# Kernel optimization log

Measured on AMD Instinct MI355X. Metric: run time of the kernel, lower is better.

## Reference

```python
import jax, jax.numpy as jnp
import numpy as np

N_NODES = 50000
N_EDGES = 800000
N_GRAPHS = 64
NEG_SLOPE = 0.2  # PyG GATConv default leaky_relu slope
EPS = 1e-16      # PyG softmax denominator epsilon


def gat_conv(x, W, a_src, a_dst, bias, src, dst, n_nodes):
    """PyG GATConv (heads=1, concat=True, self-loops already appended).
    x: [N, F_in], W: [F_in, H*F], a_src/a_dst: [H, F], bias: [H*F]."""
    H, F = a_src.shape
    h = (x @ W).reshape(-1, H, F)                      # [N, H, F]
    alpha_src = jnp.einsum('nhf,hf->nh', h, a_src)     # [N, H]
    alpha_dst = jnp.einsum('nhf,hf->nh', h, a_dst)     # [N, H]
    e = jax.nn.leaky_relu(alpha_src[src] + alpha_dst[dst], NEG_SLOPE)  # [E, H]
    # segment softmax over incoming edges of each destination node
    e_max = jax.ops.segment_max(e, dst, num_segments=n_nodes)          # [N, H]
    e_exp = jnp.exp(e - e_max[dst])
    denom = jax.ops.segment_sum(e_exp, dst, num_segments=n_nodes)      # [N, H]
    alpha = e_exp / (denom[dst] + EPS)                                 # [E, H]
    msg = alpha[:, :, None] * h[src]                                   # [E, H, F]
    out = jax.ops.segment_sum(msg, dst, num_segments=n_nodes)          # [N, H, F]
    return out.reshape(-1, H * F) + bias


def global_mean_pool(x, batch, n_graphs):
    s = jax.ops.segment_sum(x, batch, num_segments=n_graphs)
    cnt = jax.ops.segment_sum(jnp.ones((x.shape[0],), x.dtype), batch, num_segments=n_graphs)
    return s / jnp.maximum(cnt, 1.0)[:, None]


def setup_inputs() -> dict:
    key = jax.random.key(0)
    ks = jax.random.split(key, 10)
    d_in, d_h, d_out, L, H = 128, 128, 10, 3, 1
    x = jax.random.normal(ks[0], (N_NODES, d_in), dtype=jnp.float32)
    edge_index = jax.random.randint(ks[1], (2, N_EDGES), 0, N_NODES, dtype=jnp.int32)
    edge_attr = jax.random.normal(ks[2], (N_EDGES, 4), dtype=jnp.float32)
    batch = jnp.sort(jax.random.randint(ks[3], (N_NODES,), 0, N_GRAPHS, dtype=jnp.int32))
    s0 = 1.0 / np.sqrt(d_in)
    sh = 1.0 / np.sqrt(d_h)
    return {
        'x': x,
        'edge_index': edge_index,
        'edge_attr': edge_attr,
        'batch': batch,
        'W0': jax.random.normal(ks[4], (d_in, d_h), dtype=jnp.float32) * s0,
        'b0': jnp.zeros((d_h,), jnp.float32),
        'Wc': jax.random.normal(ks[5], (L, d_h, H * d_h), dtype=jnp.float32) * sh,
        'att_src': jax.random.normal(ks[6], (L, H, d_h), dtype=jnp.float32) * sh,
        'att_dst': jax.random.normal(ks[7], (L, H, d_h), dtype=jnp.float32) * sh,
        'bc': jnp.zeros((L, H * d_h), jnp.float32),
        'W1': jax.random.normal(ks[8], (d_h, d_out), dtype=jnp.float32) * sh,
        'b1': jnp.zeros((d_out,), jnp.float32),
    }


def reference(x, edge_index, edge_attr, batch, W0, b0, Wc, att_src, att_dst, bc, W1, b1):
    n = x.shape[0]
    # GATConv default add_self_loops=True
    loops = jnp.arange(n, dtype=edge_index.dtype)
    src = jnp.concatenate([edge_index[0], loops])
    dst = jnp.concatenate([edge_index[1], loops])
    # dropout p=0 / eval mode -> identity
    h = jax.nn.relu(x @ W0 + b0)
    for i in range(Wc.shape[0]):
        h = jax.nn.relu(gat_conv(h, Wc[i], att_src[i], att_dst[i], bc[i], src, dst, n))
    pooled = global_mean_pool(h, batch, N_GRAPHS)   # [B, d_h]
    return pooled @ W1 + b1                          # [B, d_out]
```

## Files before the change

kernel.cpp:

```cpp
#include <hip/hip_runtime.h>
#include <hip/hip_bf16.h>
#include <hip/hip_fp16.h>
#include <hip/hip_fp8.h>

#define NN 50000
#define NE 800000
#define NG 64
#define DH 128

#define SEG 64
#define GEMMB 512
#define GEMMW (GEMMB * 4)
#define CST 136
#define CSTB 136
#define SMEM_BYTES 17408
#define NPAIR (NN / 2)
#define WTB 256
#define INITB ((NN + 255) / 256)
#define EPT 8
#define SCATB ((NE + 256 * EPT - 1) / (256 * EPT))

#if defined(__has_builtin)
# if __has_builtin(__builtin_amdgcn_cvt_pk_f32_fp8) && __has_builtin(__builtin_amdgcn_cvt_pk_fp8_f32)
#  define HW_FP8 1
# endif
#endif

typedef __bf16 bfx8 __attribute__((ext_vector_type(8)));
typedef float  f32x4 __attribute__((ext_vector_type(4)));
typedef float  f32x8 __attribute__((ext_vector_type(8)));

__device__ __forceinline__ ushort f2b(float f) {
    unsigned b = __float_as_uint(f);
    b += 0x7fff + ((b >> 16) & 1);
    return (ushort)(b >> 16);
}
__device__ __forceinline__ float b2f(ushort s) {
    return __uint_as_float((unsigned)s << 16);
}
__device__ __forceinline__ unsigned pk2(float a, float b) {
    return (unsigned)f2b(a) | ((unsigned)f2b(b) << 16);
}

__device__ __forceinline__ unsigned f2fp8(float v) {
    v = fminf(fmaxf(v, -448.f), 448.f);
#ifdef HW_FP8
    return (unsigned)__builtin_amdgcn_cvt_pk_fp8_f32(v, v, 0, false) & 0xFFu;
#else
    __hip_fp8_e4m3 t(v);
    return (unsigned)*(const unsigned char*)&t;
#endif
}
__device__ __forceinline__ void fp8x4_up(unsigned u, float* o) {
#ifdef HW_FP8
    auto lo = __builtin_amdgcn_cvt_pk_f32_fp8((int)u, false);
    auto hi = __builtin_amdgcn_cvt_pk_f32_fp8((int)u, true);
    o[0] = lo[0]; o[1] = lo[1]; o[2] = hi[0]; o[3] = hi[1];
#else
    #pragma unroll
    for (int k = 0; k < 4; ++k) {
        unsigned char c = (u >> (8 * k)) & 0xFF;
        o[k] = float(*(const __hip_fp8_e4m3*)&c);
    }
#endif
}

__launch_bounds__(256)
__global__ void k_misc(const float* __restrict__ W0, const float* __restrict__ Wc,
                       ushort* __restrict__ Wt, int* __restrict__ cur,
                       ushort* __restrict__ csr) {
    int t = threadIdx.x;
    if (blockIdx.x < WTB) {
        int i = blockIdx.x * 256 + t;
        int m = i >> 14;
        int r = i & 16383;
        int k = r >> 7, n = r & 127;
        const float* src = (m == 0) ? W0 : (Wc + (size_t)(m - 1) * DH * DH);
        Wt[(size_t)m * DH * DH + n * DH + k] = f2b(src[r]);
        return;
    }
    int n = (blockIdx.x - WTB) * 256 + t;
    if (n < NN) {
        cur[n] = (n << 6) + 1;
        csr[(size_t)n << 6] = (ushort)n;
    }
}

__launch_bounds__(256)
__global__ void k_scatter(const int* __restrict__ ei, int* __restrict__ cur,
                          ushort* __restrict__ csr) {
    int base = blockIdx.x * (256 * EPT) + threadIdx.x;
    int d[EPT], s[EPT], slot[EPT];
    #pragma unroll
    for (int j = 0; j < EPT; ++j) {
        int e = base + j * 256;
        d[j] = (e < NE) ? ei[NE + e] : -1;
    }
    #pragma unroll
    for (int j = 0; j < EPT; ++j) {
        int e = base + j * 256;
        s[j] = (e < NE) ? ei[e] : 0;
    }
    #pragma unroll
    for (int j = 0; j < EPT; ++j)
        if (d[j] >= 0) slot[j] = atomicAdd(&cur[d[j]], 1);
    #pragma unroll
    for (int j = 0; j < EPT; ++j)
        if (d[j] >= 0 && slot[j] < (d[j] << 6) + SEG) csr[slot[j]] = (ushort)s[j];
}

template<bool AF32, bool DOTS, bool OUTFP8>
__device__ __forceinline__ void gemm_body(char* smem, int gblk,
        const void* __restrict__ Av, const ushort* __restrict__ Wt,
        const float* __restrict__ bias, void* __restrict__ C, int relu,
        const float* __restrict__ avs, const float* __restrict__ avd,
        float* __restrict__ asrc, float* __restrict__ adst) {
    const int NT = NN / 16;
    int tid = threadIdx.x;
    int lane = tid & 63;
    int mrow = lane & 15;
    int quad = lane >> 4;
    int wid = (gblk * 256 + tid) >> 6;

    bfx8 b[4][8];
    #pragma unroll
    for (int ks = 0; ks < 4; ++ks) {
        int k0 = ks * 32 + quad * 8;
        #pragma unroll
        for (int t = 0; t < 8; ++t)
            b[ks][t] = *(const bfx8*)(Wt + (size_t)(t * 16 + mrow) * DH + k0);
    }
    float av[8], dv[8];
    if (DOTS) {
        #pragma unroll
        for (int t = 0; t < 8; ++t) {
            av[t] = avs[t * 16 + mrow];
            dv[t] = avd[t * 16 + mrow];
        }
    }

    for (int tile = wid; tile < NT; tile += GEMMW) {
        int row0 = tile * 16;
        int arow = row0 + mrow;

        bfx8 a[4];
        if (AF32) {
            f32x8 af[4];
            #pragma unroll
            for (int ks = 0; ks < 4; ++ks)
                af[ks] = *(const f32x8*)((const float*)Av + (size_t)arow * DH + ks * 32 + quad * 8);
            #pragma unroll
            for (int ks = 0; ks < 4; ++ks) {
                union { ushort s[8]; bfx8 v; } u;
                #pragma unroll
                for (int j = 0; j < 8; ++j) u.s[j] = f2b(af[ks][j]);
                a[ks] = u.v;
            }
        } else {
            #pragma unroll
            for (int ks = 0; ks < 4; ++ks)
                a[ks] = *(const bfx8*)((const ushort*)Av + (size_t)arow * DH + ks * 32 + quad * 8);
        }

        f32x4 acc[8];
        #pragma unroll
        for (int t = 0; t < 8; ++t)
            #pragma unroll
            for (int r = 0; r < 4; ++r) acc[t][r] = 0.f;

        #pragma unroll
        for (int ks = 0; ks < 4; ++ks)
            #pragma unroll
            for (int t = 0; t < 8; ++t)
                acc[t] = __builtin_amdgcn_mfma_f32_16x16x32_bf16(a[ks], b[ks][t], acc[t], 0, 0, 0);

        if (OUTFP8) {
            uchar* my = (uchar*)smem + (tid >> 6) * 16 * CSTB;
            #pragma unroll
            for (int t = 0; t < 8; ++t) {
                int col = t * 16 + mrow;
                float bv = bias ? bias[col] : 0.f;
                #pragma unroll
                for (int r = 0; r < 4; ++r) {
                    float v = acc[t][r] + bv;
                    if (relu) v = fmaxf(v, 0.f);
                    my[(quad * 4 + r) * CSTB + col] = (uchar)f2fp8(v);
                }
            }
            #pragma unroll
            for (int i = 0; i < 4; ++i) {
                int idx = i * 64 + lane;
                int row = idx >> 4;
                int c8 = idx & 15;
                uint2 u = *(const uint2*)(my + row * CSTB + c8 * 8);
                *(uint2*)((uchar*)C + (size_t)(row0 + row) * DH + c8 * 8) = u;
            }
        } else {
            ushort* my = (ushort*)smem + (tid >> 6) * 16 * CST;
            #pragma unroll
            for (int t = 0; t < 8; ++t) {
                int col = t * 16 + mrow;
                float bv = bias ? bias[col] : 0.f;
                #pragma unroll
                for (int r = 0; r < 4; ++r) {
                    float v = acc[t][r] + bv;
                    if (relu) v = fmaxf(v, 0.f);
                    my[(quad * 4 + r) * CST + col] = f2b(v);
                }
            }
            #pragma unroll
            for (int i = 0; i < 4; ++i) {
                int idx = i * 64 + lane;
                int row = idx >> 4;
                int c16 = idx & 15;
                uint4 u = *(const uint4*)(my + row * CST + c16 * 8);
                *(uint4*)((ushort*)C + (size_t)(row0 + row) * DH + c16 * 8) = u;
            }
        }

        if (DOTS) {
            int orow = row0 + quad * 4;
            #pragma unroll
            for (int r = 0; r < 4; ++r) {
                float ps = 0.f, pd = 0.f;
                #pragma unroll
                for (int t = 0; t < 8; ++t) {
                    ps += acc[t][r] * av[t];
                    pd += acc[t][r] * dv[t];
                }
                #pragma unroll
                for (int off = 1; off < 16; off <<= 1) {
                    ps += __shfl_xor(ps, off);
                    pd += __shfl_xor(pd, off);
                }
                if (mrow == 0) {
                    asrc[orow + r] = ps;
                    adst[orow + r] = pd;
                }
            }
        }
    }
}

__launch_bounds__(256)
__global__ void k_gemm1(const float* __restrict__ x, const ushort* __restrict__ Wt,
                        const float* __restrict__ b0, ushort* __restrict__ hB) {
    __shared__ char smem[SMEM_BYTES];
    gemm_body<true, false, false>(smem, blockIdx.x, x, Wt, b0, hB, 1,
                                  nullptr, nullptr, nullptr, nullptr);
}

__launch_bounds__(256)
__global__ void k_gemmdots(const ushort* __restrict__ hB, const ushort* __restrict__ Wt,
                           uchar* __restrict__ hA,
                           const float* __restrict__ avs, const float* __restrict__ avd,
                           float* __restrict__ asrc, float* __restrict__ adst) {
    __shared__ char smem[SMEM_BYTES];
    gemm_body<false, true, true>(smem, blockIdx.x, hB, Wt, nullptr, hA, 0,
                                 avs, avd, asrc, adst);
}

__device__ __forceinline__ void aggr_one(int wid, int lane,
        const uchar* __restrict__ h8, const float* __restrict__ asrc,
        const float* __restrict__ adst, const int* __restrict__ cur,
        const ushort* __restrict__ csr,
        const float* __restrict__ bias, ushort* __restrict__ hout) {
    int start = wid << 6;
    int cnt = min(cur[wid] - start, SEG);
    float ad = adst[wid];

    int s = csr[start + lane];
    float e = -1e30f;
    if (lane < cnt) {
        float t = asrc[s] + ad;
        e = fmaxf(t, 0.f) + 0.2f * fminf(t, 0.f);
    }
    float m = e;
    #pragma unroll
    for (int off = 32; off; off >>= 1) m = fmaxf(m, __shfl_xor(m, off));
    float w = (lane < cnt) ? __expf(e - m) : 0.f;
    float dsum = w;
    #pragma unroll
    for (int off = 32; off; off >>= 1) dsum += __shfl_xor(dsum, off);

    int g = lane >> 4, fidx = lane & 15;
    float acc[8];
    #pragma unroll
    for (int k = 0; k < 8; ++k) acc[k] = 0.f;

    int steps = (cnt + 3) >> 2;
    const uint2* hp = (const uint2*)h8;
    for (int j = 0; j < steps; ++j) {
        int e0 = j * 4 + g;
        float w0 = __shfl(w, e0);
        int   s0 = __shfl(s, e0);
        uint2 u0 = hp[(size_t)s0 * 16 + fidx];
        float v[8];
        fp8x4_up(u0.x, v); fp8x4_up(u0.y, v + 4);
        #pragma unroll
        for (int k = 0; k < 8; ++k) acc[k] += w0 * v[k];
    }
    #pragma unroll
    for (int k = 0; k < 8; ++k) {
        acc[k] += __shfl_xor(acc[k], 16);
        acc[k] += __shfl_xor(acc[k], 32);
    }
    if (g == 0) {
        float inv = 1.f / (dsum + 1e-16f);
        const float4* bp = (const float4*)bias;
        float4 b0 = bp[fidx * 2], b1 = bp[fidx * 2 + 1];
        uint4 o;
        o.x = pk2(fmaxf(acc[0] * inv + b0.x, 0.f), fmaxf(acc[1] * inv + b0.y, 0.f));
        o.y = pk2(fmaxf(acc[2] * inv + b0.z, 0.f), fmaxf(acc[3] * inv + b0.w, 0.f));
        o.z = pk2(fmaxf(acc[4] * inv + b1.x, 0.f), fmaxf(acc[5] * inv + b1.y, 0.f));
        o.w = pk2(fmaxf(acc[6] * inv + b1.z, 0.f), fmaxf(acc[7] * inv + b1.w, 0.f));
        ((uint4*)hout)[(size_t)wid * 16 + fidx] = o;
    }
}

__launch_bounds__(256)
__global__ void k_aggr(const uchar* __restrict__ h8, const float* __restrict__ asrc,
                       const float* __restrict__ adst, const int* __restrict__ cur,
                       const ushort* __restrict__ csr,
                       const float* __restrict__ bias, ushort* __restrict__ hout) {
    int pid = (blockIdx.x * blockDim.x + threadIdx.x) >> 6;
    int lane = threadIdx.x & 63;
    if (pid >= NPAIR) return;
    int half = lane >> 5, hl = lane & 31;
    int nd = pid * 2 + half;
    int start = nd << 6;

    int cnt = min(cur[nd] - start, SEG);
    int cother = __shfl_xor(cnt, 32);
    if (max(cnt, cother) <= 32) {
        float ad = adst[nd];
        int s = csr[start + hl];
        float e = -1e30f;
        if (hl < cnt) {
            float t = asrc[s] + ad;
            e = fmaxf(t, 0.f) + 0.2f * fminf(t, 0.f);
        }
        float m = e;
        #pragma unroll
        for (int off = 16; off; off >>= 1) m = fmaxf(m, __shfl_xor(m, off));
        float w = (hl < cnt) ? __expf(e - m) : 0.f;
        float dsum = w;
        #pragma unroll
        for (int off = 16; off; off >>= 1) dsum += __shfl_xor(dsum, off);

        int g = hl >> 4, fidx = hl & 15;
        int lbase = half * 32;
        float acc[8];
        #pragma unroll
        for (int k = 0; k < 8; ++k) acc[k] = 0.f;

        int steps = (cnt + 1) >> 1;
        const uint2* hp = (const uint2*)h8;
        int j = 0;
        for (; j + 3 < steps; j += 4) {
            int   e0 = j * 2 + g,       e1 = e0 + 2, e2 = e0 + 4, e3 = e0 + 6;
            float w0 = __shfl(w, lbase + e0), w1 = __shfl(w, lbase + e1);
            float w2 = __shfl(w, lbase + e2), w3 = __shfl(w, lbase + e3);
            int   s0 = __shfl(s, lbase + e0), s1 = __shfl(s, lbase + e1);
            int   s2 = __shfl(s, lbase + e2), s3 = __shfl(s, lbase + e3);
            uint2 u0 = hp[(size_t)s0 * 16 + fidx];
            uint2 u1 = hp[(size_t)s1 * 16 + fidx];
            uint2 u2 = hp[(size_t)s2 * 16 + fidx];
            uint2 u3 = hp[(size_t)s3 * 16 + fidx];
            float v[8];
            fp8x4_up(u0.x, v); fp8x4_up(u0.y, v + 4);
            #pragma unroll
            for (int k = 0; k < 8; ++k) acc[k] += w0 * v[k];
            fp8x4_up(u1.x, v); fp8x4_up(u1.y, v + 4);
            #pragma unroll
            for (int k = 0; k < 8; ++k) acc[k] += w1 * v[k];
            fp8x4_up(u2.x, v); fp8x4_up(u2.y, v + 4);
            #pragma unroll
            for (int k = 0; k < 8; ++k) acc[k] += w2 * v[k];
            fp8x4_up(u3.x, v); fp8x4_up(u3.y, v + 4);
            #pragma unroll
            for (int k = 0; k < 8; ++k) acc[k] += w3 * v[k];
        }
        for (; j < steps; ++j) {
            int   e0 = j * 2 + g;
            float w0 = __shfl(w, lbase + e0);
            int   s0 = __shfl(s, lbase + e0);
            uint2 u0 = hp[(size_t)s0 * 16 + fidx];
            float v[8];
            fp8x4_up(u0.x, v); fp8x4_up(u0.y, v + 4);
            #pragma unroll
            for (int k = 0; k < 8; ++k) acc[k] += w0 * v[k];
        }
        #pragma unroll
        for (int k = 0; k < 8; ++k) acc[k] += __shfl_xor(acc[k], 16);
        if (g == 0) {
            float inv = 1.f / (dsum + 1e-16f);
            const float4* bp = (const float4*)bias;
            float4 b0 = bp[fidx * 2], b1 = bp[fidx * 2 + 1];
            uint4 o;
            o.x = pk2(fmaxf(acc[0] * inv + b0.x, 0.f), fmaxf(acc[1] * inv + b0.y, 0.f));
            o.y = pk2(fmaxf(acc[2] * inv + b0.z, 0.f), fmaxf(acc[3] * inv + b0.w, 0.f));
            o.z = pk2(fmaxf(acc[4] * inv + b1.x, 0.f), fmaxf(acc[5] * inv + b1.y, 0.f));
            o.w = pk2(fmaxf(acc[6] * inv + b1.z, 0.f), fmaxf(acc[7] * inv + b1.w, 0.f));
            ((uint4*)hout)[(size_t)nd * 16 + fidx] = o;
        }
        return;
    }

    aggr_one(pid * 2,     lane, h8, asrc, adst, cur, csr, bias, hout);
    aggr_one(pid * 2 + 1, lane, h8, asrc, adst, cur, csr, bias, hout);
}

__launch_bounds__(256)
__global__ void k_pool(const ushort* __restrict__ h, const int* __restrict__ batch,
                       float* __restrict__ gsum, int* __restrict__ gcnt) {
    int slot = threadIdx.x >> 7;
    int f = threadIdx.x & 127;
    int n0 = blockIdx.x * 64;
    int n1 = min(n0 + 64, NN);
    int first = n0 + slot;
    if (first >= n1) return;
    int g0 = batch[n0], g1 = batch[n1 - 1];
    if (g0 == g1) {
        float acc = 0.f;
        for (int nd = first; nd < n1; nd += 2)
            acc += b2f(h[(size_t)nd * DH + f]);
        atomicAdd(&gsum[g0 * DH + f], acc);
        if (f == 0 && slot == 0) atomicAdd(&gcnt[g0], n1 - n0);
        return;
    }
    float acc = 0.f; int run = 0;
    int gcur = batch[first];
    for (int nd = first; nd < n1; nd += 2) {
        int g = batch[nd];
        if (g != gcur) {
            atomicAdd(&gsum[gcur * DH + f], acc);
            if (f == 0) atomicAdd(&gcnt[gcur], run);
            acc = 0.f; run = 0; gcur = g;
        }
        acc += b2f(h[(size_t)nd * DH + f]);
        run += 1;
    }
    atomicAdd(&gsum[gcur * DH + f], acc);
    if (f == 0) atomicAdd(&gcnt[gcur], run);
}

__global__ void k_final(const float* __restrict__ gsum, const int* __restrict__ gcnt,
                        const float* __restrict__ W1, const float* __restrict__ b1,
                        float* __restrict__ out) {
    int t = threadIdx.x;
    if (t >= NG * 10) return;
    int g = t / 10, o = t % 10;
    float inv = 1.f / fmaxf((float)gcnt[g], 1.f);
    float acc = 0.f;
    for (int f = 0; f < DH; ++f) acc += gsum[g * DH + f] * W1[f * 10 + o];
    out[t] = acc * inv + b1[o];
}

extern "C" void kernel_launch(void* const* d_in, const int* in_sizes, int n_in,
                              void* d_out, int out_size, void* d_ws, size_t ws_size,
                              hipStream_t stream) {
    const float* x       = (const float*)d_in[0];
    const int*   ei      = (const int*)d_in[1];
    const int*   batch   = (const int*)d_in[3];
    const float* W0      = (const float*)d_in[4];
    const float* b0      = (const float*)d_in[5];
    const float* Wc      = (const float*)d_in[6];
    const float* att_src = (const float*)d_in[7];
    const float* att_dst = (const float*)d_in[8];
    const float* bc      = (const float*)d_in[9];
    const float* W1      = (const float*)d_in[10];
    const float* b1      = (const float*)d_in[11];
    float* out = (float*)d_out;

    char* ws = (char*)d_ws;
    size_t off = 0;
    auto alloc = [&](size_t bytes) {
        void* p = ws + off;
        off += (bytes + 255) & ~(size_t)255;
        return p;
    };
    uchar*    hA     = (uchar*)alloc((size_t)NN * DH);
    ushort*   hB     = (ushort*)alloc((size_t)NN * DH * 2);
    ushort*   Wt     = (ushort*)alloc((size_t)4 * DH * DH * 2);
    ushort*   csr    = (ushort*)alloc((size_t)NN * SEG * 2);
    int*      cur    = (int*)alloc((size_t)NN * 4);
    float*    asrc   = (float*)alloc(NN * 4);
    float*    adst   = (float*)alloc(NN * 4);
    float*    gsum   = (float*)alloc(NG * DH * 4);
    int*      gcnt   = (int*)alloc(NG * 4);

    hipMemsetAsync(csr, 0, (size_t)NN * SEG * 2, stream);
    hipMemsetAsync(gsum, 0, NG * DH * 4 + 256, stream);

    k_misc<<<WTB + INITB, 256, 0, stream>>>(W0, Wc, Wt, cur, csr);
    k_scatter<<<SCATB, 256, 0, stream>>>(ei, cur, csr);
    k_gemm1<<<GEMMB, 256, 0, stream>>>(x, Wt, b0, hB);

    for (int l = 0; l < 3; ++l) {
        k_gemmdots<<<GEMMB, 256, 0, stream>>>(hB, Wt + (size_t)(l + 1) * DH * DH, hA,
                                              att_src + l * DH, att_dst + l * DH,
                                              asrc, adst);
        k_aggr<<<(NPAIR + 3) / 4, 256, 0, stream>>>(hA, asrc, adst, cur, csr,
                                                    bc + l * DH, hB);
    }

    k_pool<<<(NN + 63) / 64, 256, 0, stream>>>(hB, batch, gsum, gcnt);
    k_final<<<1, NG * 10, 0, stream>>>(gsum, gcnt, W1, b1, out);
}
```

Before: 306.1 us.

## Fuse front-end init, scatter and first GEMM into one kernel; deepen gather unroll

Merges weight conversion, self-loop init, edge scatter and the first GEMM into a single launch with block-range dispatch. It removes the dependency on a cur-init pass by zeroing cur via memset and storing relative slots. The first GEMM converts fp32 W0 on the fly with strided loads. The aggregation gather loop gains an 8-wide unrolled batch to issue more loads in flight, at the cost of more registers.

```diff
diff --git a/kernel.cpp b/kernel.cpp
--- a/kernel.cpp
+++ b/kernel.cpp
@@ -15,10 +15,11 @@
 #define CSTB 136
 #define SMEM_BYTES 17408
 #define NPAIR (NN / 2)
-#define WTB 256
-#define INITB ((NN + 255) / 256)
 #define EPT 8
 #define SCATB ((NE + 256 * EPT - 1) / (256 * EPT))
+#define WCB 192
+#define INITB ((NN + 255) / 256)
+#define FRONTB (SCATB + GEMMB + WCB + INITB)
 
 #if defined(__has_builtin)
 # if __has_builtin(__builtin_amdgcn_cvt_pk_f32_fp8) && __has_builtin(__builtin_amdgcn_cvt_pk_fp8_f32)
@@ -65,53 +66,9 @@
 #endif
 }
 
-__launch_bounds__(256)
-__global__ void k_misc(const float* __restrict__ W0, const float* __restrict__ Wc,
-                       ushort* __restrict__ Wt, int* __restrict__ cur,
-                       ushort* __restrict__ csr) {
-    int t = threadIdx.x;
-    if (blockIdx.x < WTB) {
-        int i = blockIdx.x * 256 + t;
-        int m = i >> 14;
-        int r = i & 16383;
-        int k = r >> 7, n = r & 127;
-        const float* src = (m == 0) ? W0 : (Wc + (size_t)(m - 1) * DH * DH);
-        Wt[(size_t)m * DH * DH + n * DH + k] = f2b(src[r]);
-        return;
-    }
-    int n = (blockIdx.x - WTB) * 256 + t;
-    if (n < NN) {
-        cur[n] = (n << 6) + 1;
-        csr[(size_t)n << 6] = (ushort)n;
-    }
-}
-
-__launch_bounds__(256)
-__global__ void k_scatter(const int* __restrict__ ei, int* __restrict__ cur,
-                          ushort* __restrict__ csr) {
-    int base = blockIdx.x * (256 * EPT) + threadIdx.x;
-    int d[EPT], s[EPT], slot[EPT];
-    #pragma unroll
-    for (int j = 0; j < EPT; ++j) {
-        int e = base + j * 256;
-        d[j] = (e < NE) ? ei[NE + e] : -1;
-    }
-    #pragma unroll
-    for (int j = 0; j < EPT; ++j) {
-        int e = base + j * 256;
-        s[j] = (e < NE) ? ei[e] : 0;
-    }
-    #pragma unroll
-    for (int j = 0; j < EPT; ++j)
-        if (d[j] >= 0) slot[j] = atomicAdd(&cur[d[j]], 1);
-    #pragma unroll
-    for (int j = 0; j < EPT; ++j)
-        if (d[j] >= 0 && slot[j] < (d[j] << 6) + SEG) csr[slot[j]] = (ushort)s[j];
-}
-
-template<bool AF32, bool DOTS, bool OUTFP8>
+template<bool AF32, bool BF32, bool DOTS, bool OUTFP8>
 __device__ __forceinline__ void gemm_body(char* smem, int gblk,
-        const void* __restrict__ Av, const ushort* __restrict__ Wt,
+        const void* __restrict__ Av, const void* __restrict__ Wp,
         const float* __restrict__ bias, void* __restrict__ C, int relu,
         const float* __restrict__ avs, const float* __restrict__ avd,
         float* __restrict__ asrc, float* __restrict__ adst) {
@@ -123,12 +80,29 @@
     int wid = (gblk * 256 + tid) >> 6;
 
     bfx8 b[4][8];
-    #pragma unroll
-    for (int ks = 0; ks < 4; ++ks) {
-        int k0 = ks * 32 + quad * 8;
-        #pragma unroll
-        for (int t = 0; t < 8; ++t)
-            b[ks][t] = *(const bfx8*)(Wt + (size_t)(t * 16 + mrow) * DH + k0);
+    if (BF32) {
+        const float* W = (const float*)Wp;
+        #pragma unroll
+        for (int ks = 0; ks < 4; ++ks) {
+            int k0 = ks * 32 + quad * 8;
+            #pragma unroll
+            for (int t = 0; t < 8; ++t) {
+                int n = t * 16 + mrow;
+                union { ushort s[8]; bfx8 v; } u;
+                #pragma unroll
+                for (int j = 0; j < 8; ++j) u.s[j] = f2b(W[(size_t)(k0 + j) * DH + n]);
+                b[ks][t] = u.v;
+            }
+        }
+    } else {
+        const ushort* Wt = (const ushort*)Wp;
+        #pragma unroll
+        for (int ks = 0; ks < 4; ++ks) {
+            int k0 = ks * 32 + quad * 8;
+            #pragma unroll
+            for (int t = 0; t < 8; ++t)
+                b[ks][t] = *(const bfx8*)(Wt + (size_t)(t * 16 + mrow) * DH + k0);
+        }
     }
     float av[8], dv[8];
     if (DOTS) {
@@ -243,11 +217,51 @@
 }
 
 __launch_bounds__(256)
-__global__ void k_gemm1(const float* __restrict__ x, const ushort* __restrict__ Wt,
+__global__ void k_front(const int* __restrict__ ei, int* __restrict__ cur,
+                        ushort* __restrict__ csr,
+                        const float* __restrict__ Wc, ushort* __restrict__ Wt,
+                        const float* __restrict__ x, const float* __restrict__ W0,
                         const float* __restrict__ b0, ushort* __restrict__ hB) {
     __shared__ char smem[SMEM_BYTES];
-    gemm_body<true, false, false>(smem, blockIdx.x, x, Wt, b0, hB, 1,
-                                  nullptr, nullptr, nullptr, nullptr);
+    int t = threadIdx.x;
+    unsigned bid = blockIdx.x;
+    if (bid < SCATB) {
+        int base = bid * (256 * EPT) + t;
+        int d[EPT], s[EPT], slot[EPT];
+        #pragma unroll
+        for (int j = 0; j < EPT; ++j) {
+            int e = base + j * 256;
+            d[j] = (e < NE) ? ei[NE + e] : -1;
+        }
+        #pragma unroll
+        for (int j = 0; j < EPT; ++j) {
+            int e = base + j * 256;
+            s[j] = (e < NE) ? ei[e] : 0;
+        }
+        #pragma unroll
+        for (int j = 0; j < EPT; ++j)
+            if (d[j] >= 0) slot[j] = atomicAdd(&cur[d[j]], 1);
+        #pragma unroll
+        for (int j = 0; j < EPT; ++j)
+            if (d[j] >= 0 && slot[j] < SEG - 1)
+                csr[((size_t)d[j] << 6) + 1 + slot[j]] = (ushort)s[j];
+        return;
+    }
+    if (bid < SCATB + GEMMB) {
+        gemm_body<true, true, false, false>(smem, bid - SCATB, x, W0, b0, hB, 1,
+                                            nullptr, nullptr, nullptr, nullptr);
+        return;
+    }
+    if (bid < SCATB + GEMMB + WCB) {
+        int i = (bid - SCATB - GEMMB) * 256 + t;
+        int m = i >> 14;
+        int r = i & 16383;
+        int k = r >> 7, n = r & 127;
+        Wt[(size_t)(m + 1) * DH * DH + n * DH + k] = f2b(Wc[(size_t)m * DH * DH + r]);
+        return;
+    }
+    int n = (bid - SCATB - GEMMB - WCB) * 256 + t;
+    if (n < NN) csr[(size_t)n << 6] = (ushort)n;
 }
 
 __launch_bounds__(256)
@@ -256,8 +270,8 @@
                            const float* __restrict__ avs, const float* __restrict__ avd,
                            float* __restrict__ asrc, float* __restrict__ adst) {
     __shared__ char smem[SMEM_BYTES];
-    gemm_body<false, true, true>(smem, blockIdx.x, hB, Wt, nullptr, hA, 0,
-                                 avs, avd, asrc, adst);
+    gemm_body<false, false, true, true>(smem, blockIdx.x, hB, Wt, nullptr, hA, 0,
+                                        avs, avd, asrc, adst);
 }
 
 __device__ __forceinline__ void aggr_one(int wid, int lane,
@@ -266,7 +280,7 @@
         const ushort* __restrict__ csr,
         const float* __restrict__ bias, ushort* __restrict__ hout) {
     int start = wid << 6;
-    int cnt = min(cur[wid] - start, SEG);
+    int cnt = min(cur[wid] + 1, SEG);
     float ad = adst[wid];
 
     int s = csr[start + lane];
@@ -330,7 +344,7 @@
     int nd = pid * 2 + half;
     int start = nd << 6;
 
-    int cnt = min(cur[nd] - start, SEG);
+    int cnt = min(cur[nd] + 1, SEG);
     int cother = __shfl_xor(cnt, 32);
     if (max(cnt, cother) <= 32) {
         float ad = adst[nd];
@@ -357,29 +371,41 @@
         int steps = (cnt + 1) >> 1;
         const uint2* hp = (const uint2*)h8;
         int j = 0;
+        for (; j + 7 < steps; j += 8) {
+            float ww[8]; int ss[8]; uint2 uu[8];
+            #pragma unroll
+            for (int q = 0; q < 8; ++q) {
+                int eq = (j + q) * 2 + g;
+                ww[q] = __shfl(w, lbase + eq);
+                ss[q] = __shfl(s, lbase + eq);
+            }
+            #pragma unroll
+            for (int q = 0; q < 8; ++q) uu[q] = hp[(size_t)ss[q] * 16 + fidx];
+            #pragma unroll
+            for (int q = 0; q < 8; ++q) {
+                float v[8];
+                fp8x4_up(uu[q].x, v); fp8x4_up(uu[q].y, v + 4);
+                #pragma unroll
+                for (int k = 0; k < 8; ++k) acc[k] += ww[q] * v[k];
+            }
+        }
         for (; j + 3 < steps; j += 4) {
-            int   e0 = j * 2 + g,       e1 = e0 + 2, e2 = e0 + 4, e3 = e0 + 6;
-            float w0 = __shfl(w, lbase + e0), w1 = __shfl(w, lbase + e1);
-            float w2 = __shfl(w, lbase + e2), w3 = __shfl(w, lbase + e3);
-            int   s0 = __shfl(s, lbase + e0), s1 = __shfl(s, lbase + e1);
-            int   s2 = __shfl(s, lbase + e2), s3 = __shfl(s, lbase + e3);
-            uint2 u0 = hp[(size_t)s0 * 16 + fidx];
-            uint2 u1 = hp[(size_t)s1 * 16 + fidx];
-            uint2 u2 = hp[(size_t)s2 * 16 + fidx];
-            uint2 u3 = hp[(size_t)s3 * 16 + fidx];
-            float v[8];
-            fp8x4_up(u0.x, v); fp8x4_up(u0.y, v + 4);
-            #pragma unroll
-            for (int k = 0; k < 8; ++k) acc[k] += w0 * v[k];
-            fp8x4_up(u1.x, v); fp8x4_up(u1.y, v + 4);
-            #pragma unroll
-            for (int k = 0; k < 8; ++k) acc[k] += w1 * v[k];
-            fp8x4_up(u2.x, v); fp8x4_up(u2.y, v + 4);
-            #pragma unroll
-            for (int k = 0; k < 8; ++k) acc[k] += w2 * v[k];
-            fp8x4_up(u3.x, v); fp8x4_up(u3.y, v + 4);
-            #pragma unroll
-            for (int k = 0; k < 8; ++k) acc[k] += w3 * v[k];
+            float ww[4]; int ss[4]; uint2 uu[4];
+            #pragma unroll
+            for (int q = 0; q < 4; ++q) {
+                int eq = (j + q) * 2 + g;
+                ww[q] = __shfl(w, lbase + eq);
+                ss[q] = __shfl(s, lbase + eq);
+            }
+            #pragma unroll
+            for (int q = 0; q < 4; ++q) uu[q] = hp[(size_t)ss[q] * 16 + fidx];
+            #pragma unroll
+            for (int q = 0; q < 4; ++q) {
+                float v[8];
+                fp8x4_up(uu[q].x, v); fp8x4_up(uu[q].y, v + 4);
+                #pragma unroll
+                for (int k = 0; k < 8; ++k) acc[k] += ww[q] * v[k];
+            }
         }
         for (; j < steps; ++j) {
             int   e0 = j * 2 + g;
@@ -490,12 +516,10 @@
     float*    gsum   = (float*)alloc(NG * DH * 4);
     int*      gcnt   = (int*)alloc(NG * 4);
 
-    hipMemsetAsync(csr, 0, (size_t)NN * SEG * 2, stream);
+    hipMemsetAsync(csr, 0, (size_t)NN * SEG * 2 + (size_t)NN * 4, stream);
     hipMemsetAsync(gsum, 0, NG * DH * 4 + 256, stream);
 
-    k_misc<<<WTB + INITB, 256, 0, stream>>>(W0, Wc, Wt, cur, csr);
-    k_scatter<<<SCATB, 256, 0, stream>>>(ei, cur, csr);
-    k_gemm1<<<GEMMB, 256, 0, stream>>>(x, Wt, b0, hB);
+    k_front<<<FRONTB, 256, 0, stream>>>(ei, cur, csr, Wc, Wt, x, W0, b0, hB);
 
     for (int l = 0; l < 3; ++l) {
         k_gemmdots<<<GEMMB, 256, 0, stream>>>(hB, Wt + (size_t)(l + 1) * DH * DH, hA,
```

After: 305.2 us. About the same (-0.3%).

## Fuse CSR init and scatter into one prep kernel; widen aggr gathers to 16B

Applied to the files above, without the earlier changes.

Merges the weight-transpose/init kernel and the edge-scatter kernel into a single launch. It does this by zeroing the per-node counters with the existing memset, so they no longer need a separate init pass, and writing edges at slot+1 after the self-loop. The aggregation fast path now has each lane load a 16-byte fp8 chunk, with 8 lanes covering a row and 4 edges processed per step, instead of 8-byte chunks. That means fewer, wider gathers but more registers and an extra shuffle reduction stage. The self-loop write and the scatter writes now run in the same kernel without ordering, though they touch disjoint slots.

```diff
diff --git a/kernel.cpp b/kernel.cpp
--- a/kernel.cpp
+++ b/kernel.cpp
@@ -15,10 +15,11 @@
 #define CSTB 136
 #define SMEM_BYTES 17408
 #define NPAIR (NN / 2)
+#define EPT 8
+#define SCATB ((NE + 256 * EPT - 1) / (256 * EPT))
 #define WTB 256
 #define INITB ((NN + 255) / 256)
-#define EPT 8
-#define SCATB ((NE + 256 * EPT - 1) / (256 * EPT))
+#define PREPB (SCATB + WTB + INITB)
 
 #if defined(__has_builtin)
 # if __has_builtin(__builtin_amdgcn_cvt_pk_f32_fp8) && __has_builtin(__builtin_amdgcn_cvt_pk_fp8_f32)
@@ -66,12 +67,36 @@
 }
 
 __launch_bounds__(256)
-__global__ void k_misc(const float* __restrict__ W0, const float* __restrict__ Wc,
-                       ushort* __restrict__ Wt, int* __restrict__ cur,
-                       ushort* __restrict__ csr) {
+__global__ void k_prep(const int* __restrict__ ei, int* __restrict__ cur,
+                       ushort* __restrict__ csr,
+                       const float* __restrict__ W0, const float* __restrict__ Wc,
+                       ushort* __restrict__ Wt) {
     int t = threadIdx.x;
-    if (blockIdx.x < WTB) {
-        int i = blockIdx.x * 256 + t;
+    unsigned bid = blockIdx.x;
+    if (bid < SCATB) {
+        int base = bid * (256 * EPT) + t;
+        int d[EPT], s[EPT], slot[EPT];
+        #pragma unroll
+        for (int j = 0; j < EPT; ++j) {
+            int e = base + j * 256;
+            d[j] = (e < NE) ? ei[NE + e] : -1;
+        }
+        #pragma unroll
+        for (int j = 0; j < EPT; ++j) {
+            int e = base + j * 256;
+            s[j] = (e < NE) ? ei[e] : 0;
+        }
+        #pragma unroll
+        for (int j = 0; j < EPT; ++j)
+            if (d[j] >= 0) slot[j] = atomicAdd(&cur[d[j]], 1);
+        #pragma unroll
+        for (int j = 0; j < EPT; ++j)
+            if (d[j] >= 0 && slot[j] < SEG - 1)
+                csr[((size_t)d[j] << 6) + 1 + slot[j]] = (ushort)s[j];
+        return;
+    }
+    if (bid < SCATB + WTB) {
+        int i = (bid - SCATB) * 256 + t;
         int m = i >> 14;
         int r = i & 16383;
         int k = r >> 7, n = r & 127;
@@ -79,34 +104,8 @@
         Wt[(size_t)m * DH * DH + n * DH + k] = f2b(src[r]);
         return;
     }
-    int n = (blockIdx.x - WTB) * 256 + t;
-    if (n < NN) {
-        cur[n] = (n << 6) + 1;
-        csr[(size_t)n << 6] = (ushort)n;
-    }
-}
-
-__launch_bounds__(256)
-__global__ void k_scatter(const int* __restrict__ ei, int* __restrict__ cur,
-                          ushort* __restrict__ csr) {
-    int base = blockIdx.x * (256 * EPT) + threadIdx.x;
-    int d[EPT], s[EPT], slot[EPT];
-    #pragma unroll
-    for (int j = 0; j < EPT; ++j) {
-        int e = base + j * 256;
-        d[j] = (e < NE) ? ei[NE + e] : -1;
-    }
-    #pragma unroll
-    for (int j = 0; j < EPT; ++j) {
-        int e = base + j * 256;
-        s[j] = (e < NE) ? ei[e] : 0;
-    }
-    #pragma unroll
-    for (int j = 0; j < EPT; ++j)
-        if (d[j] >= 0) slot[j] = atomicAdd(&cur[d[j]], 1);
-    #pragma unroll
-    for (int j = 0; j < EPT; ++j)
-        if (d[j] >= 0 && slot[j] < (d[j] << 6) + SEG) csr[slot[j]] = (ushort)s[j];
+    int n = (bid - SCATB - WTB) * 256 + t;
+    if (n < NN) csr[(size_t)n << 6] = (ushort)n;
 }
 
 template<bool AF32, bool DOTS, bool OUTFP8>
@@ -266,7 +265,7 @@
         const ushort* __restrict__ csr,
         const float* __restrict__ bias, ushort* __restrict__ hout) {
     int start = wid << 6;
-    int cnt = min(cur[wid] - start, SEG);
+    int cnt = min(cur[wid] + 1, SEG);
     float ad = adst[wid];
 
     int s = csr[start + lane];
@@ -330,7 +329,7 @@
     int nd = pid * 2 + half;
     int start = nd << 6;
 
-    int cnt = min(cur[nd] - start, SEG);
+    int cnt = min(cur[nd] + 1, SEG);
     int cother = __shfl_xor(cnt, 32);
     if (max(cnt, cother) <= 32) {
         float ad = adst[nd];
@@ -348,61 +347,66 @@
         #pragma unroll
         for (int off = 16; off; off >>= 1) dsum += __shfl_xor(dsum, off);
 
-        int g = hl >> 4, fidx = hl & 15;
+        int g = hl >> 3, fidx = hl & 7;
         int lbase = half * 32;
-        float acc[8];
-        #pragma unroll
-        for (int k = 0; k < 8; ++k) acc[k] = 0.f;
-
-        int steps = (cnt + 1) >> 1;
-        const uint2* hp = (const uint2*)h8;
+        float acc[16];
+        #pragma unroll
+        for (int k = 0; k < 16; ++k) acc[k] = 0.f;
+
+        int steps = (cnt + 3) >> 2;
+        const uint4* hp = (const uint4*)h8;
         int j = 0;
         for (; j + 3 < steps; j += 4) {
-            int   e0 = j * 2 + g,       e1 = e0 + 2, e2 = e0 + 4, e3 = e0 + 6;
-            float w0 = __shfl(w, lbase + e0), w1 = __shfl(w, lbase + e1);
-            float w2 = __shfl(w, lbase + e2), w3 = __shfl(w, lbase + e3);
-            int   s0 = __shfl(s, lbase + e0), s1 = __shfl(s, lbase + e1);
-            int   s2 = __shfl(s, lbase + e2), s3 = __shfl(s, lbase + e3);
-            uint2 u0 = hp[(size_t)s0 * 16 + fidx];
-            uint2 u1 = hp[(size_t)s1 * 16 + fidx];
-            uint2 u2 = hp[(size_t)s2 * 16 + fidx];
-            uint2 u3 = hp[(size_t)s3 * 16 + fidx];
-            float v[8];
-            fp8x4_up(u0.x, v); fp8x4_up(u0.y, v + 4);
-            #pragma unroll
-            for (int k = 0; k < 8; ++k) acc[k] += w0 * v[k];
-            fp8x4_up(u1.x, v); fp8x4_up(u1.y, v + 4);
-            #pragma unroll
-            for (int k = 0; k < 8; ++k) acc[k] += w1 * v[k];
-            fp8x4_up(u2.x, v); fp8x4_up(u2.y, v + 4);
-            #pragma unroll
-            for (int k = 0; k < 8; ++k) acc[k] += w2 * v[k];
-            fp8x4_up(u3.x, v); fp8x4_up(u3.y, v + 4);
-            #pragma unroll
-            for (int k = 0; k < 8; ++k) acc[k] += w3 * v[k];
+            float ww[4]; int ss[4]; uint4 uu[4];
+            #pragma unroll
+            for (int q = 0; q < 4; ++q) {
+                int eq = (j + q) * 4 + g;
+                ww[q] = __shfl(w, lbase + eq);
+                ss[q] = __shfl(s, lbase + eq);
+            }
+            #pragma unroll
+            for (int q = 0; q < 4; ++q) uu[q] = hp[(size_t)ss[q] * 8 + fidx];
+            #pragma unroll
+            for (int q = 0; q < 4; ++q) {
+                float v[16];
+                fp8x4_up(uu[q].x, v);      fp8x4_up(uu[q].y, v + 4);
+                fp8x4_up(uu[q].z, v + 8);  fp8x4_up(uu[q].w, v + 12);
+                #pragma unroll
+                for (int k = 0; k < 16; ++k) acc[k] += ww[q] * v[k];
+            }
         }
         for (; j < steps; ++j) {
-            int   e0 = j * 2 + g;
+            int   e0 = j * 4 + g;
             float w0 = __shfl(w, lbase + e0);
             int   s0 = __shfl(s, lbase + e0);
-            uint2 u0 = hp[(size_t)s0 * 16 + fidx];
-            float v[8];
-            fp8x4_up(u0.x, v); fp8x4_up(u0.y, v + 4);
-            #pragma unroll
-            for (int k = 0; k < 8; ++k) acc[k] += w0 * v[k];
-        }
-        #pragma unroll
-        for (int k = 0; k < 8; ++k) acc[k] += __shfl_xor(acc[k], 16);
+            uint4 u0 = hp[(size_t)s0 * 8 + fidx];
+            float v[16];
+            fp8x4_up(u0.x, v);      fp8x4_up(u0.y, v + 4);
+            fp8x4_up(u0.z, v + 8);  fp8x4_up(u0.w, v + 12);
+            #pragma unroll
+            for (int k = 0; k < 16; ++k) acc[k] += w0 * v[k];
+        }
+        #pragma unroll
+        for (int k = 0; k < 16; ++k) {
+            acc[k] += __shfl_xor(acc[k], 8);
+            acc[k] += __shfl_xor(acc[k], 16);
+        }
         if (g == 0) {
             float inv = 1.f / (dsum + 1e-16f);
             const float4* bp = (const float4*)bias;
-            float4 b0 = bp[fidx * 2], b1 = bp[fidx * 2 + 1];
-            uint4 o;
-            o.x = pk2(fmaxf(acc[0] * inv + b0.x, 0.f), fmaxf(acc[1] * inv + b0.y, 0.f));
-            o.y = pk2(fmaxf(acc[2] * inv + b0.z, 0.f), fmaxf(acc[3] * inv + b0.w, 0.f));
-            o.z = pk2(fmaxf(acc[4] * inv + b1.x, 0.f), fmaxf(acc[5] * inv + b1.y, 0.f));
-            o.w = pk2(fmaxf(acc[6] * inv + b1.z, 0.f), fmaxf(acc[7] * inv + b1.w, 0.f));
-            ((uint4*)hout)[(size_t)nd * 16 + fidx] = o;
+            float4 b0 = bp[fidx * 4], b1 = bp[fidx * 4 + 1];
+            float4 b2 = bp[fidx * 4 + 2], b3 = bp[fidx * 4 + 3];
+            uint4 o0, o1;
+            o0.x = pk2(fmaxf(acc[0] * inv + b0.x, 0.f),  fmaxf(acc[1] * inv + b0.y, 0.f));
+            o0.y = pk2(fmaxf(acc[2] * inv + b0.z, 0.f),  fmaxf(acc[3] * inv + b0.w, 0.f));
+            o0.z = pk2(fmaxf(acc[4] * inv + b1.x, 0.f),  fmaxf(acc[5] * inv + b1.y, 0.f));
+            o0.w = pk2(fmaxf(acc[6] * inv + b1.z, 0.f),  fmaxf(acc[7] * inv + b1.w, 0.f));
+            o1.x = pk2(fmaxf(acc[8] * inv + b2.x, 0.f),  fmaxf(acc[9] * inv + b2.y, 0.f));
+            o1.y = pk2(fmaxf(acc[10] * inv + b2.z, 0.f), fmaxf(acc[11] * inv + b2.w, 0.f));
+            o1.z = pk2(fmaxf(acc[12] * inv + b3.x, 0.f), fmaxf(acc[13] * inv + b3.y, 0.f));
+            o1.w = pk2(fmaxf(acc[14] * inv + b3.z, 0.f), fmaxf(acc[15] * inv + b3.w, 0.f));
+            ((uint4*)hout)[(size_t)nd * 16 + fidx * 2]     = o0;
+            ((uint4*)hout)[(size_t)nd * 16 + fidx * 2 + 1] = o1;
         }
         return;
     }
@@ -490,11 +494,10 @@
     float*    gsum   = (float*)alloc(NG * DH * 4);
     int*      gcnt   = (int*)alloc(NG * 4);
 
-    hipMemsetAsync(csr, 0, (size_t)NN * SEG * 2, stream);
+    hipMemsetAsync(csr, 0, (size_t)NN * SEG * 2 + (size_t)NN * 4, stream);
     hipMemsetAsync(gsum, 0, NG * DH * 4 + 256, stream);
 
-    k_misc<<<WTB + INITB, 256, 0, stream>>>(W0, Wc, Wt, cur, csr);
-    k_scatter<<<SCATB, 256, 0, stream>>>(ei, cur, csr);
+    k_prep<<<PREPB, 256, 0, stream>>>(ei, cur, csr, W0, Wc, Wt);
     k_gemm1<<<GEMMB, 256, 0, stream>>>(x, Wt, b0, hB);
 
     for (int l = 0; l < 3; ++l) {
```

New measurement: 312.5 us. 1.02x slower.
